# Optimization experiments

Measured on AMD Instinct MI355X. Metric: run time of the kernel, lower is better.

Reference implementation:

```python
import jax, jax.numpy as jnp
import numpy as np

B, S, E, H = 4, 2048, 768, 12
D = E // H  # 64

def setup_inputs() -> dict:
    key = jax.random.key(0)
    k1, k2, k3, k4, k5 = jax.random.split(key, 5)
    x = jax.random.normal(k1, (B, S, E), dtype=jnp.float32)
    att_mask = jnp.ones((B, S), dtype=jnp.int32)
    # parameters (stored transposed vs torch: [in, out])
    W_attn = jax.random.normal(k2, (E, 3 * E), dtype=jnp.float32) * (1.0 / np.sqrt(E))
    b_attn = jax.random.normal(k3, (3 * E,), dtype=jnp.float32) * 0.02
    W_proj = jax.random.normal(k4, (E, E), dtype=jnp.float32) * (1.0 / np.sqrt(E))
    b_proj = jax.random.normal(k5, (E,), dtype=jnp.float32) * 0.02
    return {"x": x, "W_attn": W_attn, "b_attn": b_attn,
            "W_proj": W_proj, "b_proj": b_proj, "att_mask": att_mask}

def reference(x, W_attn, b_attn, W_proj, b_proj, att_mask):
    b, s, e = x.shape
    qkv = x @ W_attn + b_attn                       # [B,S,3E]
    q, k, v = jnp.split(qkv, 3, axis=-1)
    # [B,H,S,D]
    q = q.reshape(b, s, H, D).transpose(0, 2, 1, 3)
    k = k.reshape(b, s, H, D).transpose(0, 2, 1, 3)
    v = v.reshape(b, s, H, D).transpose(0, 2, 1, 3)
    att = jnp.einsum('bhqd,bhkd->bhqk', q, k) * (1.0 / np.sqrt(D))
    causal = jnp.tril(jnp.ones((s, s), dtype=bool))          # [S,S]
    mask = causal[None, None] & (att_mask[:, None, None, :] != 0)  # [B,1,S,S]
    att = jnp.where(mask, att, -jnp.inf)
    att = jax.nn.softmax(att, axis=-1)
    y = jnp.einsum('bhqk,bhkd->bhqd', att, v)       # [B,H,S,D]
    y = y.transpose(0, 2, 1, 3).reshape(b, s, e)
    return y @ W_proj + b_proj
```

## Files before the change

kernel.cpp:

```cpp
#include <hip/hip_runtime.h>
#include <cstdint>


typedef __bf16 bf16x8 __attribute__((ext_vector_type(8)));
typedef __bf16 bf16x4 __attribute__((ext_vector_type(4)));
typedef float  f32x4  __attribute__((ext_vector_type(4)));
typedef float  f32x16 __attribute__((ext_vector_type(16)));

#define MFMA16(a, b, c) __builtin_amdgcn_mfma_f32_16x16x32_bf16(a, b, c, 0, 0, 0)
#define MFMA32(a, b, c) __builtin_amdgcn_mfma_f32_32x32x16_bf16(a, b, c, 0, 0, 0)

static constexpr int Bb = 4, Ss = 2048, Ee = 768, Hh = 12, Dd = 64;
#define QSCALE 0.18033688011112042f

__device__ __forceinline__ void gl2lds16(const void* g, void* l) {
  __builtin_amdgcn_global_load_lds(
      (const __attribute__((address_space(1))) void*)g,
      (__attribute__((address_space(3))) void*)l, 16, 0, 0);
}

__device__ __forceinline__ float fexp2(float x) {
#if __has_builtin(__builtin_amdgcn_exp2f)
  return __builtin_amdgcn_exp2f(x);
#else
  return exp2f(x);
#endif
}

__device__ __forceinline__ int swap23(int x) {
  return (x & ~12) | ((x & 4) << 1) | ((x & 8) >> 1);
}

__global__ void cast_f32_bf16(const float* __restrict__ x,
                              __bf16* __restrict__ y, int n) {
  int i = (blockIdx.x * blockDim.x + threadIdx.x) * 4;
  if (i < n) {
    float4 v = *(const float4*)(x + i);
    bf16x4 o = {(__bf16)v.x, (__bf16)v.y, (__bf16)v.z, (__bf16)v.w};
    *(bf16x4*)(y + i) = o;
  }
}

__global__ void transpose_cast(const float* __restrict__ W,
                               __bf16* __restrict__ Wt, int K, int N) {
  __shared__ float t[64][65];
  const int k0 = blockIdx.y * 64, n0 = blockIdx.x * 64;
#pragma unroll
  for (int i = 0; i < 16; ++i) {
    int lin = i * 256 + threadIdx.x;
    int r = lin >> 6, c = lin & 63;
    t[r][c] = W[(size_t)(k0 + r) * N + n0 + c];
  }
  __syncthreads();
#pragma unroll
  for (int i = 0; i < 16; ++i) {
    int lin = i * 256 + threadIdx.x;
    int r = lin >> 6, c = lin & 63;
    Wt[(size_t)(n0 + r) * K + k0 + c] = (__bf16)t[c][r];
  }
}

template <int MODE>
__global__ __launch_bounds__(256) void gemm_bt(
    const __bf16* __restrict__ A, const __bf16* __restrict__ Bt,
    const float* __restrict__ bias, __bf16* __restrict__ Qb,
    __bf16* __restrict__ Kb, __bf16* __restrict__ VTb,
    float* __restrict__ out, int K, int N) {
  __shared__ __align__(16) __bf16 As[128 * 32];
  __shared__ __align__(16) __bf16 Bs[128 * 32];
  const int tid = threadIdx.x;
  const int wave = tid >> 6, lane = tid & 63;
  const int quad = lane >> 4, c16 = lane & 15;
  const int m0 = blockIdx.y * 128, n0 = blockIdx.x * 128;
  const int wm = (wave >> 1) * 64, wn = (wave & 1) * 64;

  f32x4 acc[4][4] = {};

  for (int k0 = 0; k0 < K; k0 += 32) {
    __syncthreads();
#pragma unroll
    for (int i = 0; i < 2; ++i) {
      const int cb = (i * 4 + wave) * 64;
      const int c = cb + lane;
      const int row = c >> 2, kk = (c & 3) * 8;
      gl2lds16(&A[(size_t)(m0 + row) * K + k0 + kk], &As[cb * 8]);
      gl2lds16(&Bt[(size_t)(n0 + row) * K + k0 + kk], &Bs[cb * 8]);
    }
    __syncthreads();
    bf16x8 af[4], bf[4];
#pragma unroll
    for (int mi = 0; mi < 4; ++mi)
      af[mi] = *(const bf16x8*)&As[(wm + mi * 16 + c16) * 32 + quad * 8];
#pragma unroll
    for (int ni = 0; ni < 4; ++ni)
      bf[ni] = *(const bf16x8*)&Bs[(wn + ni * 16 + c16) * 32 + quad * 8];
#pragma unroll
    for (int mi = 0; mi < 4; ++mi)
#pragma unroll
      for (int ni = 0; ni < 4; ++ni)
        acc[mi][ni] = MFMA16(af[mi], bf[ni], acc[mi][ni]);
  }

#pragma unroll
  for (int mi = 0; mi < 4; ++mi) {
#pragma unroll
    for (int ni = 0; ni < 4; ++ni) {
      const int gcol = n0 + wn + ni * 16 + c16;
      const float bv = bias[gcol];
      const int growb = m0 + wm + mi * 16 + quad * 4;
      if (MODE == 0) {
        const int which = gcol / Ee;
        const int e = gcol - which * Ee;
        const int hh = e >> 6, dd = e & 63;
        const int bb = growb >> 11, ss = growb & 2047;
        const size_t bh = (size_t)(bb * Hh + hh);
        if (which == 2) {
          const int ssp = swap23(ss);
          bf16x4 o;
#pragma unroll
          for (int r = 0; r < 4; ++r) o[r] = (__bf16)(acc[mi][ni][r] + bv);
          *(bf16x4*)&VTb[(bh * Dd + dd) * Ss + ssp] = o;
        } else if (which == 0) {
          const int ddp = swap23(dd);
#pragma unroll
          for (int r = 0; r < 4; ++r)
            Qb[(bh * Ss + ss + r) * Dd + ddp] =
                (__bf16)((acc[mi][ni][r] + bv) * QSCALE);
        } else {
          const int ddp = swap23(dd);
#pragma unroll
          for (int r = 0; r < 4; ++r)
            Kb[(bh * Ss + ss + r) * Dd + ddp] = (__bf16)(acc[mi][ni][r] + bv);
        }
      } else {
#pragma unroll
        for (int r = 0; r < 4; ++r)
          out[(size_t)(growb + r) * N + gcol] = acc[mi][ni][r] + bv;
      }
    }
  }
}

__global__ __launch_bounds__(256, 3) void flash_attn(
    const __bf16* __restrict__ Qb, const __bf16* __restrict__ Kb,
    const __bf16* __restrict__ VTb, const int* __restrict__ amask,
    __bf16* __restrict__ Yb) {
  const int bid = blockIdx.x;
  const int xcd = bid & 7, j = bid >> 3;
  const int bh = xcd * 6 + (j >> 4);
  const int bidx = j & 15;
  const int b = bh / Hh, h = bh - b * Hh;
  const int tid = threadIdx.x, w = tid >> 6, lane = tid & 63;
  const int hl = lane >> 5, l31 = lane & 31;
  const int r7 = l31 & 7;

  const int s = ((w & 2) << 4) + ((w & 1) ? 31 - bidx : bidx);
  const int qs = s * 32;
  const int qg = qs + l31;
  const int ktmax = s >> 1;
  const int nkt = ((63 - bidx) >> 1) + 1;

  const __bf16* Qp = Qb + (size_t)bh * Ss * Dd;
  const __bf16* Kp = Kb + (size_t)bh * Ss * Dd;
  const __bf16* Vp = VTb + (size_t)bh * Dd * Ss;

  __shared__ __align__(16) __bf16 Ksh[3 * 64 * 64];
  __shared__ __align__(16) __bf16 Vsh[3 * 64 * 64];
  __shared__ uint64_t ballots[32];

  bf16x8 qf[4];
#pragma unroll
  for (int wd = 0; wd < 4; ++wd)
    qf[wd] = *(const bf16x8*)&Qp[(size_t)qg * Dd + wd * 16 + hl * 8];

#pragma unroll
  for (int i = 0; i < 8; ++i) {
    const int t = w * 8 + i;
    const uint64_t ball = __ballot(amask[b * Ss + t * 64 + lane] != 0);
    if (lane == 0) ballots[t] = ball;
  }
  asm volatile("s_waitcnt lgkmcnt(0)" ::: "memory");

  auto stage = [&](int kt, int buf) {
    __bf16* kb = &Ksh[buf * 4096];
    __bf16* vb = &Vsh[buf * 4096];
    const char* ksrc = (const char*)(Kp + (size_t)kt * 64 * Dd);
    const char* vsrc = (const char*)Vp + (size_t)kt * 128;
#pragma unroll
    for (int i = 0; i < 2; ++i) {
      const int cb = i * 256 + w * 64;
      const int p = cb + lane;
      const int row = p >> 3;
      const int cc = (p & 7) ^ (row & 7);
      gl2lds16(ksrc + (size_t)row * 128 + cc * 16, &kb[cb * 8]);
      gl2lds16(vsrc + (size_t)row * 4096 + cc * 16, &vb[cb * 8]);
    }
  };

  stage(0, 0);
  if (nkt > 1) stage(1, 1);

  f32x16 yacc[2] = {};
  float m_i = -30000.f, l_i = 0.f;

  for (int kt = 0; kt < nkt; ++kt) {
    if (kt + 1 < nkt)
      asm volatile("s_waitcnt vmcnt(4)\n\ts_barrier" ::: "memory");
    else
      asm volatile("s_waitcnt vmcnt(0)\n\ts_barrier" ::: "memory");
    if (kt + 2 < nkt) stage(kt + 2, (kt + 2) % 3);

    if (kt > ktmax) continue;
    const int k0 = kt * 64;
    const __bf16* kb = &Ksh[(kt % 3) * 4096];
    const __bf16* vb = &Vsh[(kt % 3) * 4096];

    f32x16 sg[2];
#pragma unroll
    for (int g = 0; g < 2; ++g) {
      f32x16 acc = {};
#pragma unroll
      for (int wd = 0; wd < 4; ++wd) {
        const bf16x8 kf = *(const bf16x8*)&kb[(g * 32 + l31) * 64 +
                                             (((2 * wd + hl) ^ r7) * 8)];
        acc = MFMA32(kf, qf[wd], acc);
      }
      sg[g] = acc;
    }

    if (k0 + 63 > qs) {
#pragma unroll
      for (int g = 0; g < 2; ++g)
#pragma unroll
        for (int r = 0; r < 16; ++r) {
          const int key = k0 + g * 32 + (r & 3) + 8 * (r >> 2) + 4 * hl;
          sg[g][r] = (key <= qg) ? sg[g][r] : -30000.f;
        }
    }
    const uint64_t mball = ballots[kt];
    if (mball != ~0ull) {
#pragma unroll
      for (int g = 0; g < 2; ++g)
#pragma unroll
        for (int r = 0; r < 16; ++r) {
          const int kr = g * 32 + (r & 3) + 8 * (r >> 2) + 4 * hl;
          sg[g][r] = ((mball >> kr) & 1) ? sg[g][r] : -30000.f;
        }
    }

    float mx = sg[0][0];
#pragma unroll
    for (int r = 1; r < 16; ++r) mx = fmaxf(mx, sg[0][r]);
#pragma unroll
    for (int r = 0; r < 16; ++r) mx = fmaxf(mx, sg[1][r]);
    mx = fmaxf(mx, __shfl_xor(mx, 32));
    const float mnew = fmaxf(m_i, mx);
    const float alpha = fexp2(m_i - mnew);
    float rs = 0.f;
#pragma unroll
    for (int g = 0; g < 2; ++g)
#pragma unroll
      for (int r = 0; r < 16; ++r) {
        const float e = fexp2(sg[g][r] - mnew);
        sg[g][r] = e;
        rs += e;
      }
    rs += __shfl_xor(rs, 32);
    l_i = l_i * alpha + rs;
    m_i = mnew;
#pragma unroll
    for (int dt = 0; dt < 2; ++dt)
#pragma unroll
      for (int r = 0; r < 16; ++r) yacc[dt][r] *= alpha;

    bf16x8 pf[4];
#pragma unroll
    for (int W = 0; W < 4; ++W) {
      bf16x8 f;
#pragma unroll
      for (int jj = 0; jj < 8; ++jj)
        f[jj] = (__bf16)sg[W >> 1][8 * (W & 1) + jj];
      pf[W] = f;
    }

#pragma unroll
    for (int dt = 0; dt < 2; ++dt)
#pragma unroll
      for (int W = 0; W < 4; ++W) {
        const bf16x8 vf = *(const bf16x8*)&vb[(dt * 32 + l31) * 64 +
                                             (((2 * W + hl) ^ r7) * 8)];
        yacc[dt] = MFMA32(vf, pf[W], yacc[dt]);
      }
  }

  const float inv = 1.f / l_i;
  __bf16* yrow = Yb + (size_t)(b * Ss + qg) * Ee + h * Dd;
#pragma unroll
  for (int dt = 0; dt < 2; ++dt)
#pragma unroll
    for (int sreg = 0; sreg < 4; ++sreg) {
      bf16x4 o;
#pragma unroll
      for (int r = 0; r < 4; ++r)
        o[r] = (__bf16)(yacc[dt][sreg * 4 + r] * inv);
      *(bf16x4*)&yrow[dt * 32 + sreg * 8 + hl * 4] = o;
    }
}

extern "C" void kernel_launch(void* const* d_in, const int* in_sizes, int n_in,
                              void* d_out, int out_size, void* d_ws,
                              size_t ws_size, hipStream_t stream) {
  const float* x      = (const float*)d_in[0];
  const float* W_attn = (const float*)d_in[1];
  const float* b_attn = (const float*)d_in[2];
  const float* W_proj = (const float*)d_in[3];
  const float* b_proj = (const float*)d_in[4];
  const int* att_mask = (const int*)d_in[5];
  float* out = (float*)d_out;

  char* ws = (char*)d_ws;
  __bf16* xb  = (__bf16*)(ws);
  __bf16* Wat = (__bf16*)(ws + 12582912);
  __bf16* Wpt = (__bf16*)(ws + 16121856);
  __bf16* Qb  = (__bf16*)(ws + 17301504);
  __bf16* Kb  = (__bf16*)(ws + 29884416);
  __bf16* VTb = (__bf16*)(ws + 42467328);
  __bf16* Yb  = xb;

  cast_f32_bf16<<<6144, 256, 0, stream>>>(x, xb, Bb * Ss * Ee);
  transpose_cast<<<dim3(36, 12), 256, 0, stream>>>(W_attn, Wat, Ee, 3 * Ee);
  transpose_cast<<<dim3(12, 12), 256, 0, stream>>>(W_proj, Wpt, Ee, Ee);

  gemm_bt<0><<<dim3(18, 64), 256, 0, stream>>>(xb, Wat, b_attn, Qb, Kb, VTb,
                                               nullptr, Ee, 3 * Ee);
  flash_attn<<<768, 256, 0, stream>>>(Qb, Kb, VTb, att_mask, Yb);
  gemm_bt<1><<<dim3(6, 64), 256, 0, stream>>>(Yb, Wpt, b_proj, nullptr,
                                              nullptr, nullptr, out, Ee, Ee);
}
```

Baseline: 231.5 us.

## Load K/V tiles directly to registers per wave, dropping LDS staging

The flash-attention kernel no longer stages K and V tiles into a triple-buffered LDS ring shared by the block. Each wave now loads its own K/V fragments from global memory into registers, prefetching the next tile while computing the current one. This removes the block barriers, lets each wave stop at its own causal limit, and computes the attention-mask ballot per tile instead of precomputing it. In exchange, global and L2 traffic rises because the four waves no longer share K/V loads, register pressure rises (occupancy hint lowered from 3 to 2), and the V loads are strided across rows.

```diff
diff --git a/kernel.cpp b/kernel.cpp
--- a/kernel.cpp
+++ b/kernel.cpp
@@ -141,7 +141,7 @@
   }
 }
 
-__global__ __launch_bounds__(256, 3) void flash_attn(
+__global__ __launch_bounds__(256, 2) void flash_attn(
     const __bf16* __restrict__ Qb, const __bf16* __restrict__ Kb,
     const __bf16* __restrict__ VTb, const int* __restrict__ amask,
     __bf16* __restrict__ Yb) {
@@ -152,83 +152,60 @@
   const int b = bh / Hh, h = bh - b * Hh;
   const int tid = threadIdx.x, w = tid >> 6, lane = tid & 63;
   const int hl = lane >> 5, l31 = lane & 31;
-  const int r7 = l31 & 7;
 
   const int s = ((w & 2) << 4) + ((w & 1) ? 31 - bidx : bidx);
-  const int qs = s * 32;
-  const int qg = qs + l31;
+  const int qg = s * 32 + l31;
   const int ktmax = s >> 1;
-  const int nkt = ((63 - bidx) >> 1) + 1;
 
   const __bf16* Qp = Qb + (size_t)bh * Ss * Dd;
   const __bf16* Kp = Kb + (size_t)bh * Ss * Dd;
   const __bf16* Vp = VTb + (size_t)bh * Dd * Ss;
-
-  __shared__ __align__(16) __bf16 Ksh[3 * 64 * 64];
-  __shared__ __align__(16) __bf16 Vsh[3 * 64 * 64];
-  __shared__ uint64_t ballots[32];
+  const int* amp = amask + b * Ss;
 
   bf16x8 qf[4];
 #pragma unroll
   for (int wd = 0; wd < 4; ++wd)
     qf[wd] = *(const bf16x8*)&Qp[(size_t)qg * Dd + wd * 16 + hl * 8];
 
-#pragma unroll
-  for (int i = 0; i < 8; ++i) {
-    const int t = w * 8 + i;
-    const uint64_t ball = __ballot(amask[b * Ss + t * 64 + lane] != 0);
-    if (lane == 0) ballots[t] = ball;
-  }
-  asm volatile("s_waitcnt lgkmcnt(0)" ::: "memory");
-
-  auto stage = [&](int kt, int buf) {
-    __bf16* kb = &Ksh[buf * 4096];
-    __bf16* vb = &Vsh[buf * 4096];
-    const char* ksrc = (const char*)(Kp + (size_t)kt * 64 * Dd);
-    const char* vsrc = (const char*)Vp + (size_t)kt * 128;
-#pragma unroll
-    for (int i = 0; i < 2; ++i) {
-      const int cb = i * 256 + w * 64;
-      const int p = cb + lane;
-      const int row = p >> 3;
-      const int cc = (p & 7) ^ (row & 7);
-      gl2lds16(ksrc + (size_t)row * 128 + cc * 16, &kb[cb * 8]);
-      gl2lds16(vsrc + (size_t)row * 4096 + cc * 16, &vb[cb * 8]);
-    }
+  auto loadK = [&](int kt, bf16x8* dst) {
+    const __bf16* base = Kp + (size_t)kt * 64 * Dd;
+#pragma unroll
+    for (int i = 0; i < 8; ++i)
+      dst[i] = *(const bf16x8*)&base[((i >> 2) * 32 + l31) * 64 +
+                                     (i & 3) * 16 + hl * 8];
   };
-
-  stage(0, 0);
-  if (nkt > 1) stage(1, 1);
+  auto loadV = [&](int kt, bf16x8* dst) {
+    const __bf16* base = Vp + (size_t)kt * 64;
+#pragma unroll
+    for (int i = 0; i < 8; ++i)
+      dst[i] = *(const bf16x8*)&base[(size_t)((i >> 2) * 32 + l31) * Ss +
+                                     (i & 3) * 16 + hl * 8];
+  };
+
+  bf16x8 kf[8], vf[8];
+  loadK(0, kf);
+  loadV(0, vf);
 
   f32x16 yacc[2] = {};
   float m_i = -30000.f, l_i = 0.f;
 
-  for (int kt = 0; kt < nkt; ++kt) {
-    if (kt + 1 < nkt)
-      asm volatile("s_waitcnt vmcnt(4)\n\ts_barrier" ::: "memory");
-    else
-      asm volatile("s_waitcnt vmcnt(0)\n\ts_barrier" ::: "memory");
-    if (kt + 2 < nkt) stage(kt + 2, (kt + 2) % 3);
-
-    if (kt > ktmax) continue;
+  for (int kt = 0; kt <= ktmax; ++kt) {
     const int k0 = kt * 64;
-    const __bf16* kb = &Ksh[(kt % 3) * 4096];
-    const __bf16* vb = &Vsh[(kt % 3) * 4096];
-
-    f32x16 sg[2];
+    const bool last = (kt == ktmax);
+    const uint64_t mball = __ballot(amp[k0 + lane] != 0);
+
+    f32x16 sg[2] = {};
 #pragma unroll
     for (int g = 0; g < 2; ++g) {
       f32x16 acc = {};
 #pragma unroll
-      for (int wd = 0; wd < 4; ++wd) {
-        const bf16x8 kf = *(const bf16x8*)&kb[(g * 32 + l31) * 64 +
-                                             (((2 * wd + hl) ^ r7) * 8)];
-        acc = MFMA32(kf, qf[wd], acc);
-      }
+      for (int wd = 0; wd < 4; ++wd)
+        acc = MFMA32(kf[g * 4 + wd], qf[wd], acc);
       sg[g] = acc;
     }
-
-    if (k0 + 63 > qs) {
+    if (!last) loadK(kt + 1, kf);
+
+    if (k0 + 63 > s * 32) {
 #pragma unroll
       for (int g = 0; g < 2; ++g)
 #pragma unroll
@@ -237,7 +214,6 @@
           sg[g][r] = (key <= qg) ? sg[g][r] : -30000.f;
         }
     }
-    const uint64_t mball = ballots[kt];
     if (mball != ~0ull) {
 #pragma unroll
       for (int g = 0; g < 2; ++g)
@@ -286,14 +262,13 @@
 #pragma unroll
     for (int dt = 0; dt < 2; ++dt)
 #pragma unroll
-      for (int W = 0; W < 4; ++W) {
-        const bf16x8 vf = *(const bf16x8*)&vb[(dt * 32 + l31) * 64 +
-                                             (((2 * W + hl) ^ r7) * 8)];
-        yacc[dt] = MFMA32(vf, pf[W], yacc[dt]);
-      }
-  }
-
-  const float inv = 1.f / l_i;
+      for (int W = 0; W < 4; ++W)
+        yacc[dt] = MFMA32(vf[dt * 4 + W], pf[W], yacc[dt]);
+
+    if (!last) loadV(kt + 1, vf);
+  }
+
+  const float inv = (l_i > 0.f) ? 1.f / l_i : 0.f;
   __bf16* yrow = Yb + (size_t)(b * Ss + qg) * Ee + h * Dd;
 #pragma unroll
   for (int dt = 0; dt < 2; ++dt)
```

After: 292.8 us. +26.4%, slower.
